# Kernel tuning notes

Hardware: AMD Instinct MI355X
Metric: run time of the kernel (lower is better)

## Reference

```python
import jax, jax.numpy as jnp
import numpy as np

N, F, E = 100000, 128, 1600000


def setup_inputs() -> dict:
    key = jax.random.key(0)
    ks = jax.random.split(key, 10)
    s = 1.0 / np.sqrt(F)
    return {
        "x": jax.random.normal(ks[0], (N, F), jnp.float32),
        "edge_index": jax.random.randint(ks[1], (2, E), 0, N),
        "edge_weight": jax.random.uniform(ks[2], (E,), jnp.float32),
        # EvolveGCNO initial weight (1, F, F) -> squeezed to (F, F)
        "initial_weight": jax.random.normal(ks[3], (F, F), jnp.float32) * s,
        # torch.nn.GRU(F, F) params, gate order (r, z, n)
        "gru_w_ih": jax.random.uniform(ks[4], (3 * F, F), jnp.float32, -s, s),
        "gru_w_hh": jax.random.uniform(ks[5], (3 * F, F), jnp.float32, -s, s),
        "gru_b_ih": jax.random.uniform(ks[6], (3 * F,), jnp.float32, -s, s),
        "gru_b_hh": jax.random.uniform(ks[7], (3 * F,), jnp.float32, -s, s),
        # Linear(F, 1)
        "lin_w": jax.random.uniform(ks[8], (1, F), jnp.float32, -s, s),
        "lin_b": jax.random.uniform(ks[9], (1,), jnp.float32, -s, s),
    }


def _evolve_weight(W0, w_ih, w_hh, b_ih, b_hh):
    # One GRU step: input = W0 rows (batch=F), hidden = W0 rows (first call of EvolveGCNO)
    gi = W0 @ w_ih.T + b_ih  # (F, 3F)
    gh = W0 @ w_hh.T + b_hh
    i_r, i_z, i_n = jnp.split(gi, 3, axis=-1)
    h_r, h_z, h_n = jnp.split(gh, 3, axis=-1)
    r = jax.nn.sigmoid(i_r + h_r)
    z = jax.nn.sigmoid(i_z + h_z)
    n = jnp.tanh(i_n + r * h_n)
    return (1.0 - z) * n + z * W0  # (F, F)


def reference(x, edge_index, edge_weight, initial_weight, gru_w_ih, gru_w_hh,
              gru_b_ih, gru_b_hh, lin_w, lin_b):
    W = _evolve_weight(initial_weight, gru_w_ih, gru_w_hh, gru_b_ih, gru_b_hh)
    n_nodes = x.shape[0]
    row, col = edge_index[0], edge_index[1]  # source, target
    # gcn_norm: add self loops (weight 1), sym-normalize D^-1/2 (A+I) D^-1/2
    loop = jnp.arange(n_nodes)
    row = jnp.concatenate([row, loop])
    col = jnp.concatenate([col, loop])
    w = jnp.concatenate([edge_weight, jnp.ones((n_nodes,), x.dtype)])
    deg = jax.ops.segment_sum(w, col, num_segments=n_nodes)
    dinv = jnp.where(deg > 0, jax.lax.rsqrt(deg), 0.0)
    norm = dinv[row] * w * dinv[col]  # (E+N,)
    xw = x @ W  # (N, F)
    # gather at sources, weighted scatter-add at targets
    h = jax.ops.segment_sum(norm[:, None] * xw[row], col, num_segments=n_nodes)
    h = jax.nn.relu(h)
    return (h @ lin_w.T + lin_b)[:, 0]  # (N,)
```

## Files before the change

kernel.cpp:

```cpp
#include <hip/hip_runtime.h>

#define F 128
#define DEG_SCALE 16777216.0f
#define DEG_INV   (1.0f / 16777216.0f)
#define BUCK_BITS 7
#define BUCK_COLS 128
#define CAP 2304
#define EPT 8
#define WB_STRIDE 136

typedef _Float16 half8 __attribute__((ext_vector_type(8)));
typedef float f32x4 __attribute__((ext_vector_type(4)));

__global__ __launch_bounds__(256) void init_kernel(
    int* __restrict__ cursor, int NZ, int NBUK,
    const float* __restrict__ W0, const float* __restrict__ wih,
    const float* __restrict__ whh, const float* __restrict__ bih,
    const float* __restrict__ bhh, float* __restrict__ W) {
  __shared__ float w0row[2][F];
  int b = blockIdx.x;
  if (b < NZ) {
    int i = b * 256 + threadIdx.x;
    if (i < NBUK) cursor[i] = 0;
    return;
  }
  int half = threadIdx.x >> 7;
  int j = threadIdx.x & 127;
  int i = (b - NZ) * 2 + half;
  w0row[half][j] = W0[i * F + j];
  __syncthreads();
  float ar = 0, az = 0, an = 0, br = 0, bz = 0, bn = 0;
  const float* wi_r = wih + (size_t)j * F;
  const float* wi_z = wih + (size_t)(j + F) * F;
  const float* wi_n = wih + (size_t)(j + 2 * F) * F;
  const float* wh_r = whh + (size_t)j * F;
  const float* wh_z = whh + (size_t)(j + F) * F;
  const float* wh_n = whh + (size_t)(j + 2 * F) * F;
#pragma unroll 4
  for (int k = 0; k < F; ++k) {
    float a = w0row[half][k];
    ar = fmaf(a, wi_r[k], ar);
    az = fmaf(a, wi_z[k], az);
    an = fmaf(a, wi_n[k], an);
    br = fmaf(a, wh_r[k], br);
    bz = fmaf(a, wh_z[k], bz);
    bn = fmaf(a, wh_n[k], bn);
  }
  float gr = ar + bih[j] + br + bhh[j];
  float gz = az + bih[j + F] + bz + bhh[j + F];
  float r = 1.f / (1.f + expf(-gr));
  float z = 1.f / (1.f + expf(-gz));
  float n = tanhf(an + bih[j + 2 * F] + r * (bn + bhh[j + 2 * F]));
  W[i * F + j] = (1.f - z) * n + z * w0row[half][j];
}

__global__ __launch_bounds__(1024) void bin_kernel(
    const int* __restrict__ row, const int* __restrict__ col,
    const float* __restrict__ ew, int* __restrict__ cursor,
    uint2* __restrict__ binned, int E, int NBUK) {
  __shared__ int cnt[1024];
  __shared__ int base[1024];
  int tid = threadIdx.x;
  cnt[tid] = 0;
  __syncthreads();
  int e0 = blockIdx.x * (1024 * EPT) + tid;
  int cc[EPT];
  int lrank[EPT];
#pragma unroll
  for (int k = 0; k < EPT; ++k) {
    int e = e0 + k * 1024;
    if (e < E) {
      cc[k] = col[e];
      lrank[k] = atomicAdd(&cnt[cc[k] >> BUCK_BITS], 1);
    } else cc[k] = -1;
  }
  __syncthreads();
  if (tid < NBUK) {
    int c = cnt[tid];
    base[tid] = c ? atomicAdd(&cursor[tid], c) : 0;
  }
  __syncthreads();
#pragma unroll
  for (int k = 0; k < EPT; ++k) {
    if (cc[k] >= 0) {
      int e = e0 + k * 1024;
      int b = cc[k] >> BUCK_BITS;
      int pos = base[b] + lrank[k];
      if (pos < CAP) {
        unsigned cl = (unsigned)(cc[k] & (BUCK_COLS - 1));
        binned[(size_t)b * CAP + pos] =
            make_uint2((unsigned)row[e] | (cl << 17), __float_as_uint(ew[e]));
      }
    }
  }
}

__global__ __launch_bounds__(256) void csr_kernel(
    const uint2* __restrict__ binned, const int* __restrict__ cursor,
    int* __restrict__ offs, float* __restrict__ dinv,
    uint2* __restrict__ pairs, int N, int NBUK) {
  __shared__ unsigned long long acc[BUCK_COLS];
  __shared__ float dinvL[BUCK_COLS];
  __shared__ int wbase[BUCK_COLS];
  __shared__ int sc[BUCK_COLS];
  __shared__ int wsum[4];
  int b = blockIdx.x;
  int tid = threadIdx.x;
  if (tid < BUCK_COLS) acc[tid] = 0ull;
  int partial = 0;
  for (int i = tid; i < b; i += 256) partial += cursor[i];
#pragma unroll
  for (int m = 32; m; m >>= 1) partial += __shfl_xor(partial, m);
  if ((tid & 63) == 0) wsum[tid >> 6] = partial;
  __syncthreads();
  int bstart = b * BUCK_COLS + wsum[0] + wsum[1] + wsum[2] + wsum[3];

  int cnt = cursor[b];
  if (cnt > CAP) cnt = CAP;
  const uint2* src = binned + (size_t)b * CAP;
  for (int i = tid; i < cnt; i += 256) {
    uint2 rec = src[i];
    int cl = rec.x >> 17;
    unsigned fx = (unsigned)(__uint_as_float(rec.y) * DEG_SCALE);
    atomicAdd(&acc[cl], ((unsigned long long)1 << 32) | (unsigned long long)fx);
  }
  __syncthreads();
  int node0 = b * BUCK_COLS;
  int cvt1 = 0;
  if (tid < BUCK_COLS) {
    unsigned long long pk = acc[tid];
    int node = node0 + tid;
    if (node < N) {
      cvt1 = (int)(pk >> 32) + 1;
      float deg = (float)(unsigned)(pk & 0xffffffffull) * DEG_INV;
      float dv = rsqrtf(deg + 1.0f);
      dinvL[tid] = dv;
      dinv[node] = dv;
    }
    sc[tid] = cvt1;
  }
  __syncthreads();
  for (int off = 1; off < BUCK_COLS; off <<= 1) {
    int x = 0;
    if (tid < BUCK_COLS && tid >= off) x = sc[tid - off];
    __syncthreads();
    if (tid < BUCK_COLS) sc[tid] += x;
    __syncthreads();
  }
  if (tid < BUCK_COLS) {
    int node = node0 + tid;
    if (node < N) {
      int abs0 = bstart + sc[tid] - cvt1;
      offs[node] = abs0;
      pairs[abs0] = make_uint2((unsigned)node << 8, __float_as_uint(dinvL[tid]));
      wbase[tid] = abs0 + 1;
    }
  }
  __syncthreads();
  for (int i = tid; i < cnt; i += 256) {
    uint2 rec = src[i];
    int cl = rec.x >> 17;
    unsigned r = rec.x & 0x1ffffu;
    float wp = __uint_as_float(rec.y) * dinvL[cl];
    int pos = atomicAdd(&wbase[cl], 1);
    pairs[pos] = make_uint2(r << 8, __float_as_uint(wp));
  }
}

__global__ __launch_bounds__(256) void norm_fix(
    uint2* __restrict__ pairs, const float* __restrict__ dinv,
    int* __restrict__ offs, int N, int total) {
  int i = blockIdx.x * 256 + threadIdx.x;
  if (i < total) {
    uint2 pr = pairs[i];
    float v = __uint_as_float(pr.y) * dinv[pr.x >> 8];
    pairs[i] = make_uint2(pr.x, __float_as_uint(v));
  } else if (i < total + 16) {
    pairs[i] = make_uint2(0u, 0u);
  }
  if (i == 0) offs[N] = total;
}

__global__ __launch_bounds__(256) void gemm_xw(
    const float* __restrict__ x, const float* __restrict__ W,
    _Float16* __restrict__ xwh, int N) {
  __shared__ _Float16 Wb[F * WB_STRIDE];
  int t = threadIdx.x;
  for (int idx = t; idx < F * F; idx += 256) {
    int k = idx >> 7, n = idx & 127;
    Wb[n * WB_STRIDE + k] = (_Float16)W[idx];
  }
  __syncthreads();

  int lane = t & 63, wave = t >> 6;
  int ln = lane & 15, q = lane >> 4;
  int rowb = blockIdx.x * 64 + wave * 16;
  int i = rowb + ln;
  int iclamp = (i < N) ? i : N - 1;
  const float* xp = x + (size_t)iclamp * F + q * 8;

  half8 a[4];
#pragma unroll
  for (int tt = 0; tt < 4; ++tt) {
    float4 v0 = *(const float4*)(xp + 32 * tt);
    float4 v1 = *(const float4*)(xp + 32 * tt + 4);
    half8 av;
    av[0] = (_Float16)v0.x; av[1] = (_Float16)v0.y;
    av[2] = (_Float16)v0.z; av[3] = (_Float16)v0.w;
    av[4] = (_Float16)v1.x; av[5] = (_Float16)v1.y;
    av[6] = (_Float16)v1.z; av[7] = (_Float16)v1.w;
    a[tt] = av;
  }

  f32x4 acc[8];
#pragma unroll
  for (int nt = 0; nt < 8; ++nt) acc[nt] = (f32x4){0.f, 0.f, 0.f, 0.f};

#pragma unroll
  for (int nt = 0; nt < 8; ++nt) {
#pragma unroll
    for (int tt = 0; tt < 4; ++tt) {
      half8 bfrag = *(const half8*)&Wb[(nt * 16 + ln) * WB_STRIDE + tt * 32 + q * 8];
      acc[nt] = __builtin_amdgcn_mfma_f32_16x16x32_f16(a[tt], bfrag, acc[nt], 0, 0, 0);
    }
  }

#pragma unroll
  for (int nt = 0; nt < 8; ++nt) {
#pragma unroll
    for (int r = 0; r < 4; ++r) {
      int rowi = rowb + q * 4 + r;
      if (rowi < N) xwh[(size_t)rowi * F + nt * 16 + ln] = (_Float16)acc[nt][r];
    }
  }
}

__global__ __launch_bounds__(256) void gather_out(
    const uint2* __restrict__ pairs, const int* __restrict__ offs,
    const char* __restrict__ xwb, const float* __restrict__ linw,
    const float* __restrict__ linb, float* __restrict__ out, int N) {
  int wave = threadIdx.x >> 6;
  int lane = threadIdx.x & 63;
  int node = blockIdx.x * 4 + wave;
  if (node >= N) return;
  int c = lane & 15;
  int q = lane >> 4;

  const char* xb = xwb + (c << 4);
  float acc[8];
#pragma unroll
  for (int j = 0; j < 8; ++j) acc[j] = 0.f;

  int start = offs[node], end = offs[node + 1];
  for (int it = start + q; it < end; it += 16) {
    uint2 p0 = pairs[it];
    uint2 p1 = pairs[it + 4];
    uint2 p2 = pairs[it + 8];
    uint2 p3 = pairs[it + 12];
    float n0 = __uint_as_float(p0.y);
    float n1 = (it + 4 < end) ? __uint_as_float(p1.y) : 0.f;
    float n2 = (it + 8 < end) ? __uint_as_float(p2.y) : 0.f;
    float n3 = (it + 12 < end) ? __uint_as_float(p3.y) : 0.f;
    half8 x0 = *(const half8*)(xb + p0.x);
    half8 x1 = *(const half8*)(xb + p1.x);
    half8 x2 = *(const half8*)(xb + p2.x);
    half8 x3 = *(const half8*)(xb + p3.x);
#pragma unroll
    for (int j = 0; j < 8; ++j) acc[j] = fmaf(n0, (float)x0[j], acc[j]);
#pragma unroll
    for (int j = 0; j < 8; ++j) acc[j] = fmaf(n1, (float)x1[j], acc[j]);
#pragma unroll
    for (int j = 0; j < 8; ++j) acc[j] = fmaf(n2, (float)x2[j], acc[j]);
#pragma unroll
    for (int j = 0; j < 8; ++j) acc[j] = fmaf(n3, (float)x3[j], acc[j]);
  }

#pragma unroll
  for (int j = 0; j < 8; ++j) {
    acc[j] += __shfl_xor(acc[j], 16);
    acc[j] += __shfl_xor(acc[j], 32);
  }

  const float4* lw4 = (const float4*)linw;
  float4 la = lw4[c * 2];
  float4 lb = lw4[c * 2 + 1];
  float p = fmaxf(acc[0], 0.f) * la.x + fmaxf(acc[1], 0.f) * la.y +
            fmaxf(acc[2], 0.f) * la.z + fmaxf(acc[3], 0.f) * la.w +
            fmaxf(acc[4], 0.f) * lb.x + fmaxf(acc[5], 0.f) * lb.y +
            fmaxf(acc[6], 0.f) * lb.z + fmaxf(acc[7], 0.f) * lb.w;
#pragma unroll
  for (int m = 8; m; m >>= 1) p += __shfl_xor(p, m);

  if (lane == 0) out[node] = p + linb[0];
}

extern "C" void kernel_launch(void* const* d_in, const int* in_sizes, int n_in,
                              void* d_out, int out_size, void* d_ws, size_t ws_size,
                              hipStream_t stream) {
  const float* x    = (const float*)d_in[0];
  const int*   ei   = (const int*)d_in[1];
  const float* ew   = (const float*)d_in[2];
  const float* W0   = (const float*)d_in[3];
  const float* wih  = (const float*)d_in[4];
  const float* whh  = (const float*)d_in[5];
  const float* bih  = (const float*)d_in[6];
  const float* bhh  = (const float*)d_in[7];
  const float* linw = (const float*)d_in[8];
  const float* linb = (const float*)d_in[9];

  int N = in_sizes[0] / F;
  int E = in_sizes[2];
  const int* row = ei;
  const int* col = ei + E;
  int NBUK = (N + BUCK_COLS - 1) / BUCK_COLS;
  int total = E + N;

  char* p = (char*)d_ws;
  auto alloc = [&](size_t bytes) {
    char* q = p;
    p += (bytes + 255) & ~(size_t)255;
    return q;
  };
  float*    W      = (float*)alloc((size_t)F * F * 4);
  int*      cursor = (int*)alloc((size_t)NBUK * 4);
  float*    dinv   = (float*)alloc((size_t)N * 4);
  int*      offs   = (int*)alloc(((size_t)N + 1) * 4);
  uint2*    binned = (uint2*)alloc((size_t)NBUK * CAP * 8);
  uint2*    pairs  = (uint2*)alloc(((size_t)total + 16) * 8);
  _Float16* xwh    = (_Float16*)alloc((size_t)N * F * 2);

  int NZ = (NBUK + 255) / 256;
  init_kernel<<<NZ + 64, 256, 0, stream>>>(cursor, NZ, NBUK, W0, wih, whh, bih, bhh, W);

  int EPB = 1024 * EPT;
  bin_kernel<<<(E + EPB - 1) / EPB, 1024, 0, stream>>>(row, col, ew, cursor, binned,
                                                       E, NBUK);
  csr_kernel<<<NBUK, 256, 0, stream>>>(binned, cursor, offs, dinv, pairs, N, NBUK);
  norm_fix<<<(total + 16 + 255) / 256, 256, 0, stream>>>(pairs, dinv, offs, N, total);

  gemm_xw<<<(N + 63) / 64, 256, 0, stream>>>(x, W, xwh, N);
  gather_out<<<(N + 3) / 4, 256, 0, stream>>>(pairs, offs, (const char*)xwh,
                                              linw, linb, (float*)d_out, N);
}
```

Measured before the change: 254.4 us.

## Fuse GEMM with edge binning and fold norm_fix into gather

Merges the xW GEMM and edge-binning kernels into one launch whose blocks are interleaved 2:1 between the two roles, so the two independent stages can overlap on the GPU. Drops the norm_fix pass by applying the source-side dinv inside gather_out, and moves the offs[N] write into init_kernel. The gather loop now clamps out-of-range pair indices instead of relying on zero padding, and accumulates with packed float2 FMAs. The trade-off is an extra random dinv load per edge in the gather, and binning now runs in 256-thread blocks with a larger shared-memory footprint per block.

```diff
diff --git a/kernel.cpp b/kernel.cpp
--- a/kernel.cpp
+++ b/kernel.cpp
@@ -11,17 +11,20 @@
 
 typedef _Float16 half8 __attribute__((ext_vector_type(8)));
 typedef float f32x4 __attribute__((ext_vector_type(4)));
+typedef float f32x2 __attribute__((ext_vector_type(2)));
 
 __global__ __launch_bounds__(256) void init_kernel(
     int* __restrict__ cursor, int NZ, int NBUK,
     const float* __restrict__ W0, const float* __restrict__ wih,
     const float* __restrict__ whh, const float* __restrict__ bih,
-    const float* __restrict__ bhh, float* __restrict__ W) {
+    const float* __restrict__ bhh, float* __restrict__ W,
+    int* __restrict__ offs, int N, int total) {
   __shared__ float w0row[2][F];
   int b = blockIdx.x;
   if (b < NZ) {
     int i = b * 256 + threadIdx.x;
     if (i < NBUK) cursor[i] = 0;
+    if (b == 0 && threadIdx.x == 0) offs[N] = total;
     return;
   }
   int half = threadIdx.x >> 7;
@@ -54,43 +57,104 @@
   W[i * F + j] = (1.f - z) * n + z * w0row[half][j];
 }
 
-__global__ __launch_bounds__(1024) void bin_kernel(
-    const int* __restrict__ row, const int* __restrict__ col,
+__global__ __launch_bounds__(256) void gemm_bin(
+    const float* __restrict__ x, const float* __restrict__ W,
+    _Float16* __restrict__ xwh, int N, int NG,
+    const int* __restrict__ erow, const int* __restrict__ ecol,
     const float* __restrict__ ew, int* __restrict__ cursor,
-    uint2* __restrict__ binned, int E, int NBUK) {
-  __shared__ int cnt[1024];
-  __shared__ int base[1024];
-  int tid = threadIdx.x;
-  cnt[tid] = 0;
-  __syncthreads();
-  int e0 = blockIdx.x * (1024 * EPT) + tid;
-  int cc[EPT];
-  int lrank[EPT];
-#pragma unroll
-  for (int k = 0; k < EPT; ++k) {
-    int e = e0 + k * 1024;
-    if (e < E) {
-      cc[k] = col[e];
-      lrank[k] = atomicAdd(&cnt[cc[k] >> BUCK_BITS], 1);
-    } else cc[k] = -1;
-  }
-  __syncthreads();
-  if (tid < NBUK) {
-    int c = cnt[tid];
-    base[tid] = c ? atomicAdd(&cursor[tid], c) : 0;
-  }
-  __syncthreads();
-#pragma unroll
-  for (int k = 0; k < EPT; ++k) {
-    if (cc[k] >= 0) {
-      int e = e0 + k * 1024;
-      int b = cc[k] >> BUCK_BITS;
-      int pos = base[b] + lrank[k];
-      if (pos < CAP) {
-        unsigned cl = (unsigned)(cc[k] & (BUCK_COLS - 1));
-        binned[(size_t)b * CAP + pos] =
-            make_uint2((unsigned)row[e] | (cl << 17), __float_as_uint(ew[e]));
+    uint2* __restrict__ binned, int E, int NBUK, int NBIN) {
+  __shared__ __align__(16) char smem[F * WB_STRIDE * 2];
+  int bi = blockIdx.x;
+  if (bi % 3 == 2) {
+    int bb = bi / 3;
+    if (bb >= NBIN) return;
+    int* cnt = (int*)smem;
+    int* base = cnt + 1024;
+    int tid = threadIdx.x;
+#pragma unroll
+    for (int u = tid; u < 1024; u += 256) cnt[u] = 0;
+    __syncthreads();
+    int e0 = bb * (256 * EPT) + tid;
+    int cc[EPT];
+    int lrank[EPT];
+#pragma unroll
+    for (int k = 0; k < EPT; ++k) {
+      int e = e0 + k * 256;
+      if (e < E) {
+        cc[k] = ecol[e];
+        lrank[k] = atomicAdd(&cnt[cc[k] >> BUCK_BITS], 1);
+      } else cc[k] = -1;
+    }
+    __syncthreads();
+    for (int u = tid; u < NBUK; u += 256) {
+      int cu = cnt[u];
+      base[u] = cu ? atomicAdd(&cursor[u], cu) : 0;
+    }
+    __syncthreads();
+#pragma unroll
+    for (int k = 0; k < EPT; ++k) {
+      if (cc[k] >= 0) {
+        int e = e0 + k * 256;
+        int bk = cc[k] >> BUCK_BITS;
+        int pos = base[bk] + lrank[k];
+        if (pos < CAP) {
+          unsigned cl = (unsigned)(cc[k] & (BUCK_COLS - 1));
+          binned[(size_t)bk * CAP + pos] =
+              make_uint2((unsigned)erow[e] | (cl << 17), __float_as_uint(ew[e]));
+        }
       }
+    }
+    return;
+  }
+  int g = (bi / 3) * 2 + (bi % 3);
+  if (g >= NG) return;
+  _Float16* Wb = (_Float16*)smem;
+  int t = threadIdx.x;
+  for (int idx = t; idx < F * F; idx += 256) {
+    int k = idx >> 7, n = idx & 127;
+    Wb[n * WB_STRIDE + k] = (_Float16)W[idx];
+  }
+  __syncthreads();
+
+  int lane = t & 63, wave = t >> 6;
+  int ln = lane & 15, q = lane >> 4;
+  int rowb = g * 64 + wave * 16;
+  int i = rowb + ln;
+  int iclamp = (i < N) ? i : N - 1;
+  const float* xp = x + (size_t)iclamp * F + q * 8;
+
+  half8 a[4];
+#pragma unroll
+  for (int tt = 0; tt < 4; ++tt) {
+    float4 v0 = *(const float4*)(xp + 32 * tt);
+    float4 v1 = *(const float4*)(xp + 32 * tt + 4);
+    half8 av;
+    av[0] = (_Float16)v0.x; av[1] = (_Float16)v0.y;
+    av[2] = (_Float16)v0.z; av[3] = (_Float16)v0.w;
+    av[4] = (_Float16)v1.x; av[5] = (_Float16)v1.y;
+    av[6] = (_Float16)v1.z; av[7] = (_Float16)v1.w;
+    a[tt] = av;
+  }
+
+  f32x4 acc[8];
+#pragma unroll
+  for (int nt = 0; nt < 8; ++nt) acc[nt] = (f32x4){0.f, 0.f, 0.f, 0.f};
+
+#pragma unroll
+  for (int nt = 0; nt < 8; ++nt) {
+#pragma unroll
+    for (int tt = 0; tt < 4; ++tt) {
+      half8 bfrag = *(const half8*)&Wb[(nt * 16 + ln) * WB_STRIDE + tt * 32 + q * 8];
+      acc[nt] = __builtin_amdgcn_mfma_f32_16x16x32_f16(a[tt], bfrag, acc[nt], 0, 0, 0);
+    }
+  }
+
+#pragma unroll
+  for (int nt = 0; nt < 8; ++nt) {
+#pragma unroll
+    for (int r = 0; r < 4; ++r) {
+      int rowi = rowb + q * 4 + r;
+      if (rowi < N) xwh[(size_t)rowi * F + nt * 16 + ln] = (_Float16)acc[nt][r];
     }
   }
 }
@@ -167,78 +231,11 @@
   }
 }
 
-__global__ __launch_bounds__(256) void norm_fix(
-    uint2* __restrict__ pairs, const float* __restrict__ dinv,
-    int* __restrict__ offs, int N, int total) {
-  int i = blockIdx.x * 256 + threadIdx.x;
-  if (i < total) {
-    uint2 pr = pairs[i];
-    float v = __uint_as_float(pr.y) * dinv[pr.x >> 8];
-    pairs[i] = make_uint2(pr.x, __float_as_uint(v));
-  } else if (i < total + 16) {
-    pairs[i] = make_uint2(0u, 0u);
-  }
-  if (i == 0) offs[N] = total;
-}
-
-__global__ __launch_bounds__(256) void gemm_xw(
-    const float* __restrict__ x, const float* __restrict__ W,
-    _Float16* __restrict__ xwh, int N) {
-  __shared__ _Float16 Wb[F * WB_STRIDE];
-  int t = threadIdx.x;
-  for (int idx = t; idx < F * F; idx += 256) {
-    int k = idx >> 7, n = idx & 127;
-    Wb[n * WB_STRIDE + k] = (_Float16)W[idx];
-  }
-  __syncthreads();
-
-  int lane = t & 63, wave = t >> 6;
-  int ln = lane & 15, q = lane >> 4;
-  int rowb = blockIdx.x * 64 + wave * 16;
-  int i = rowb + ln;
-  int iclamp = (i < N) ? i : N - 1;
-  const float* xp = x + (size_t)iclamp * F + q * 8;
-
-  half8 a[4];
-#pragma unroll
-  for (int tt = 0; tt < 4; ++tt) {
-    float4 v0 = *(const float4*)(xp + 32 * tt);
-    float4 v1 = *(const float4*)(xp + 32 * tt + 4);
-    half8 av;
-    av[0] = (_Float16)v0.x; av[1] = (_Float16)v0.y;
-    av[2] = (_Float16)v0.z; av[3] = (_Float16)v0.w;
-    av[4] = (_Float16)v1.x; av[5] = (_Float16)v1.y;
-    av[6] = (_Float16)v1.z; av[7] = (_Float16)v1.w;
-    a[tt] = av;
-  }
-
-  f32x4 acc[8];
-#pragma unroll
-  for (int nt = 0; nt < 8; ++nt) acc[nt] = (f32x4){0.f, 0.f, 0.f, 0.f};
-
-#pragma unroll
-  for (int nt = 0; nt < 8; ++nt) {
-#pragma unroll
-    for (int tt = 0; tt < 4; ++tt) {
-      half8 bfrag = *(const half8*)&Wb[(nt * 16 + ln) * WB_STRIDE + tt * 32 + q * 8];
-      acc[nt] = __builtin_amdgcn_mfma_f32_16x16x32_f16(a[tt], bfrag, acc[nt], 0, 0, 0);
-    }
-  }
-
-#pragma unroll
-  for (int nt = 0; nt < 8; ++nt) {
-#pragma unroll
-    for (int r = 0; r < 4; ++r) {
-      int rowi = rowb + q * 4 + r;
-      if (rowi < N) xwh[(size_t)rowi * F + nt * 16 + ln] = (_Float16)acc[nt][r];
-    }
-  }
-}
-
 __global__ __launch_bounds__(256) void gather_out(
     const uint2* __restrict__ pairs, const int* __restrict__ offs,
-    const char* __restrict__ xwb, const float* __restrict__ linw,
-    const float* __restrict__ linb, float* __restrict__ out, int N) {
+    const float* __restrict__ dinv, const char* __restrict__ xwb,
+    const float* __restrict__ linw, const float* __restrict__ linb,
+    float* __restrict__ out, int N) {
   int wave = threadIdx.x >> 6;
   int lane = threadIdx.x & 63;
   int node = blockIdx.x * 4 + wave;
@@ -247,47 +244,66 @@
   int q = lane >> 4;
 
   const char* xb = xwb + (c << 4);
-  float acc[8];
-#pragma unroll
-  for (int j = 0; j < 8; ++j) acc[j] = 0.f;
+  f32x2 acc[4];
+#pragma unroll
+  for (int j = 0; j < 4; ++j) acc[j] = (f32x2){0.f, 0.f};
 
   int start = offs[node], end = offs[node + 1];
   for (int it = start + q; it < end; it += 16) {
+    int i1 = (it + 4 < end) ? it + 4 : it;
+    int i2 = (it + 8 < end) ? it + 8 : it;
+    int i3 = (it + 12 < end) ? it + 12 : it;
     uint2 p0 = pairs[it];
-    uint2 p1 = pairs[it + 4];
-    uint2 p2 = pairs[it + 8];
-    uint2 p3 = pairs[it + 12];
-    float n0 = __uint_as_float(p0.y);
-    float n1 = (it + 4 < end) ? __uint_as_float(p1.y) : 0.f;
-    float n2 = (it + 8 < end) ? __uint_as_float(p2.y) : 0.f;
-    float n3 = (it + 12 < end) ? __uint_as_float(p3.y) : 0.f;
+    uint2 p1 = pairs[i1];
+    uint2 p2 = pairs[i2];
+    uint2 p3 = pairs[i3];
+    float n0 = __uint_as_float(p0.y) * dinv[p0.x >> 8];
+    float n1 = (it + 4 < end) ? __uint_as_float(p1.y) * dinv[p1.x >> 8] : 0.f;
+    float n2 = (it + 8 < end) ? __uint_as_float(p2.y) * dinv[p2.x >> 8] : 0.f;
+    float n3 = (it + 12 < end) ? __uint_as_float(p3.y) * dinv[p3.x >> 8] : 0.f;
     half8 x0 = *(const half8*)(xb + p0.x);
     half8 x1 = *(const half8*)(xb + p1.x);
     half8 x2 = *(const half8*)(xb + p2.x);
     half8 x3 = *(const half8*)(xb + p3.x);
-#pragma unroll
-    for (int j = 0; j < 8; ++j) acc[j] = fmaf(n0, (float)x0[j], acc[j]);
-#pragma unroll
-    for (int j = 0; j < 8; ++j) acc[j] = fmaf(n1, (float)x1[j], acc[j]);
-#pragma unroll
-    for (int j = 0; j < 8; ++j) acc[j] = fmaf(n2, (float)x2[j], acc[j]);
-#pragma unroll
-    for (int j = 0; j < 8; ++j) acc[j] = fmaf(n3, (float)x3[j], acc[j]);
-  }
-
+    f32x2 nv0 = {n0, n0}, nv1 = {n1, n1}, nv2 = {n2, n2}, nv3 = {n3, n3};
+#pragma unroll
+    for (int j = 0; j < 4; ++j) {
+      f32x2 v; v[0] = (float)x0[2 * j]; v[1] = (float)x0[2 * j + 1];
+      acc[j] += nv0 * v;
+    }
+#pragma unroll
+    for (int j = 0; j < 4; ++j) {
+      f32x2 v; v[0] = (float)x1[2 * j]; v[1] = (float)x1[2 * j + 1];
+      acc[j] += nv1 * v;
+    }
+#pragma unroll
+    for (int j = 0; j < 4; ++j) {
+      f32x2 v; v[0] = (float)x2[2 * j]; v[1] = (float)x2[2 * j + 1];
+      acc[j] += nv2 * v;
+    }
+#pragma unroll
+    for (int j = 0; j < 4; ++j) {
+      f32x2 v; v[0] = (float)x3[2 * j]; v[1] = (float)x3[2 * j + 1];
+      acc[j] += nv3 * v;
+    }
+  }
+
+  float a8[8];
+#pragma unroll
+  for (int j = 0; j < 8; ++j) a8[j] = acc[j >> 1][j & 1];
 #pragma unroll
   for (int j = 0; j < 8; ++j) {
-    acc[j] += __shfl_xor(acc[j], 16);
-    acc[j] += __shfl_xor(acc[j], 32);
+    a8[j] += __shfl_xor(a8[j], 16);
+    a8[j] += __shfl_xor(a8[j], 32);
   }
 
   const float4* lw4 = (const float4*)linw;
   float4 la = lw4[c * 2];
   float4 lb = lw4[c * 2 + 1];
-  float p = fmaxf(acc[0], 0.f) * la.x + fmaxf(acc[1], 0.f) * la.y +
-            fmaxf(acc[2], 0.f) * la.z + fmaxf(acc[3], 0.f) * la.w +
-            fmaxf(acc[4], 0.f) * lb.x + fmaxf(acc[5], 0.f) * lb.y +
-            fmaxf(acc[6], 0.f) * lb.z + fmaxf(acc[7], 0.f) * lb.w;
+  float p = fmaxf(a8[0], 0.f) * la.x + fmaxf(a8[1], 0.f) * la.y +
+            fmaxf(a8[2], 0.f) * la.z + fmaxf(a8[3], 0.f) * la.w +
+            fmaxf(a8[4], 0.f) * lb.x + fmaxf(a8[5], 0.f) * lb.y +
+            fmaxf(a8[6], 0.f) * lb.z + fmaxf(a8[7], 0.f) * lb.w;
 #pragma unroll
   for (int m = 8; m; m >>= 1) p += __shfl_xor(p, m);
 
@@ -330,15 +346,18 @@
   _Float16* xwh    = (_Float16*)alloc((size_t)N * F * 2);
 
   int NZ = (NBUK + 255) / 256;
-  init_kernel<<<NZ + 64, 256, 0, stream>>>(cursor, NZ, NBUK, W0, wih, whh, bih, bhh, W);
-
-  int EPB = 1024 * EPT;
-  bin_kernel<<<(E + EPB - 1) / EPB, 1024, 0, stream>>>(row, col, ew, cursor, binned,
-                                                       E, NBUK);
+  init_kernel<<<NZ + 64, 256, 0, stream>>>(cursor, NZ, NBUK, W0, wih, whh, bih, bhh,
+                                           W, offs, N, total);
+
+  int NG = (N + 63) / 64;
+  int NBIN = (E + 256 * EPT - 1) / (256 * EPT);
+  int half_g = (NG + 1) / 2;
+  int G3 = NBIN > half_g ? NBIN : half_g;
+  gemm_bin<<<3 * G3, 256, 0, stream>>>(x, W, xwh, N, NG, row, col, ew, cursor,
+                                       binned, E, NBUK, NBIN);
+
   csr_kernel<<<NBUK, 256, 0, stream>>>(binned, cursor, offs, dinv, pairs, N, NBUK);
-  norm_fix<<<(total + 16 + 255) / 256, 256, 0, stream>>>(pairs, dinv, offs, N, total);
-
-  gemm_xw<<<(N + 63) / 64, 256, 0, stream>>>(x, W, xwh, N);
-  gather_out<<<(N + 3) / 4, 256, 0, stream>>>(pairs, offs, (const char*)xwh,
+
+  gather_out<<<(N + 3) / 4, 256, 0, stream>>>(pairs, offs, dinv, (const char*)xwh,
                                               linw, linb, (float*)d_out, N);
 }
```

After: 259.7 us. 1.02x slower.
